# Optimization experiments

Hardware: AMD Instinct MI355X
Metric: run time of the kernel (lower is better)

## Reference

```python
import jax, jax.numpy as jnp
import numpy as np

# Ragged layout: 8 sequences packed into total_tokens=6144 tokens.
_SEQLENS = [1024, 512, 1024, 256, 768, 1024, 512, 1024]
_TOTAL = sum(_SEQLENS)  # 6144
_H, _D = 16, 128
_MAXLEN = 1024


def setup_inputs() -> dict:
    key = jax.random.key(0)
    kq, kk, kv = jax.random.split(key, 3)
    cu = jnp.asarray(np.concatenate([[0], np.cumsum(_SEQLENS)]), dtype=jnp.int32)
    return {
        "q": jax.random.normal(kq, (_TOTAL, _H, _D), dtype=jnp.float32),
        "k": jax.random.normal(kk, (_TOTAL, _H, _D), dtype=jnp.float32),
        "v": jax.random.normal(kv, (_TOTAL, _H, _D), dtype=jnp.float32),
        "cu_seqlens_q": cu,
        "cu_seqlens_k": cu,
        "max_seqlen_q": _MAXLEN,
        "max_seqlen_k": _MAXLEN,
    }


def _pad_gather(x, cu, L):
    """Gather packed [T,h,d] into padded [B,L,h,d] plus validity mask [B,L]."""
    starts = cu[:-1]                                   # [B]
    lens = cu[1:] - cu[:-1]                            # [B]
    pos = jnp.arange(L, dtype=cu.dtype)                # [L]
    idx = starts[:, None] + pos[None, :]               # [B,L]
    mask = pos[None, :] < lens[:, None]                # [B,L]
    idx = jnp.clip(idx, 0, x.shape[0] - 1)
    return x[idx], mask, jnp.where(mask, idx, x.shape[0])


def reference(q, k, v, cu_seqlens_q, cu_seqlens_k, max_seqlen_q, max_seqlen_k):
    # Equivalent to pytorch_varlen_attention: per-sequence SDPA (non-causal,
    # no dropout), vectorized via pad-to-max + key masking.
    T, h, d = q.shape
    qp, mq, idx_q = _pad_gather(q, cu_seqlens_q, max_seqlen_q)  # [B,Lq,h,d]
    kp, mk, _ = _pad_gather(k, cu_seqlens_k, max_seqlen_k)      # [B,Lk,h,d]
    vp, _, _ = _pad_gather(v, cu_seqlens_k, max_seqlen_k)

    scale = 1.0 / jnp.sqrt(jnp.asarray(d, dtype=q.dtype))
    scores = jnp.einsum("bqhd,bkhd->bhqk", qp, kp) * scale      # [B,h,Lq,Lk]
    neg = jnp.asarray(jnp.finfo(scores.dtype).min, scores.dtype)
    scores = jnp.where(mk[:, None, None, :], scores, neg)
    attn = jax.nn.softmax(scores, axis=-1)
    out_pad = jnp.einsum("bhqk,bkhd->bqhd", attn, vp)           # [B,Lq,h,d]

    # Scatter valid rows back to packed layout; invalid rows dropped (idx==T).
    out = jnp.zeros((T, h, d), dtype=q.dtype)
    out = out.at[idx_q.reshape(-1)].set(
        out_pad.reshape(-1, h, d), mode="drop")
    return out
```

## Files before the change

### kernel.cpp

```cpp
#include <hip/hip_runtime.h>
#include <hip/hip_bf16.h>
#include <stdint.h>

#define H 16
#define D 128
#define BM 128
#define BN 64
#define NW 4
#define NT 256

typedef __bf16 bf16_t;
typedef bf16_t bf16x8 __attribute__((ext_vector_type(8)));
typedef bf16_t bf16x2 __attribute__((ext_vector_type(2)));
typedef float f32x16 __attribute__((ext_vector_type(16)));

#define MFMA32(a, b, c) __builtin_amdgcn_mfma_f32_32x32x16_bf16(a, b, c, 0, 0, 0)

union FragU { uint32_t w[4]; bf16x8 v; };

static __device__ __forceinline__ uint32_t cvtpk_bf16(float lo, float hi) {
  uint32_t r;
  asm("v_cvt_pk_bf16_f32 %0, %1, %2" : "=v"(r) : "v"(lo), "v"(hi));
  return r;
}

static __device__ __forceinline__ void gld_lds16(const bf16_t* g, bf16_t* l) {
  __builtin_amdgcn_global_load_lds(
      (const __attribute__((address_space(1))) void*)g,
      (__attribute__((address_space(3))) void*)l, 16, 0, 0);
}


__global__ void conv_k(const float* __restrict__ kin, bf16_t* __restrict__ kb, int n8) {
  int i = blockIdx.x * blockDim.x + threadIdx.x;
  int stride = gridDim.x * blockDim.x;
  for (; i < n8; i += stride) {
    const float* p = kin + (size_t)i * 8;
    float4 a = *(const float4*)p, b = *(const float4*)(p + 4);
    bf16x8 w;
    w[0] = (bf16_t)a.x; w[1] = (bf16_t)a.y; w[2] = (bf16_t)a.z; w[3] = (bf16_t)a.w;
    w[4] = (bf16_t)b.x; w[5] = (bf16_t)b.y; w[6] = (bf16_t)b.z; w[7] = (bf16_t)b.w;
    *(bf16x8*)(kb + (size_t)i * 8) = w;
  }
}

__global__ void conv_vt(const float* __restrict__ v, bf16_t* __restrict__ vt,
                        const int* __restrict__ cuk, int nseq) {
  int tile = blockIdx.x, h = blockIdx.y;
  int acc = 0, seq = -1, lt = 0, s0k = 0, Lk = 0;
  for (int s = 0; s < nseq; ++s) {
    int a = cuk[s], b = cuk[s + 1];
    int Ls = b - a;
    int nt = (Ls + 63) / 64;
    if (tile < acc + nt) { seq = s; lt = tile - acc; s0k = a; Lk = Ls; break; }
    acc += nt;
  }
  if (seq < 0) return;
  int kv0 = lt * 64;
  int d = threadIdx.x;
  bf16x8 w[8];
  #pragma unroll
  for (int j = 0; j < 64; ++j) {
    int kv = kv0 + j; if (kv >= Lk) kv = Lk - 1;
    float val = v[((size_t)(s0k + kv) * H + h) * D + d];
    w[j >> 3][j & 7] = (bf16_t)val;
  }
  bf16_t* row = vt + (size_t)s0k * H * D + ((size_t)h * D + d) * Lk + kv0;
  #pragma unroll
  for (int i = 0; i < 8; ++i) *(bf16x8*)(row + i * 8) = w[i];
}


__global__ __launch_bounds__(NT, 2)
void fa_varlen3(const float* __restrict__ q,
                const bf16_t* __restrict__ kb,
                const bf16_t* __restrict__ vt,
                const int* __restrict__ cuq,
                const int* __restrict__ cuk,
                float* __restrict__ out,
                int nseq)
{
  __shared__ alignas(16) bf16_t sK[2][BN * D];
  __shared__ alignas(16) bf16_t sVt[2][D * BN];
  __shared__ float sRed[NW * 32];

  const int tile = blockIdx.x;
  const int h = blockIdx.y;

  int acc = 0, seq = -1, lt = 0, s0q = 0, s0k = 0, Lq = 0, Lk = 0;
  for (int s = 0; s < nseq; ++s) {
    int a = cuq[s], b = cuq[s + 1];
    int Ls = b - a;
    int nt = (Ls + BM - 1) / BM;
    if (tile < acc + nt) {
      seq = s; lt = tile - acc; s0q = a; Lq = Ls;
      s0k = cuk[s]; Lk = cuk[s + 1] - s0k;
      break;
    }
    acc += nt;
  }
  if (seq < 0) return;

  const int q0 = lt * BM;
  const int tid = threadIdx.x;
  const int warp = tid >> 6;
  const int lane = tid & 63;
  const int lq = lane & 31;
  const int hi = lane >> 5;

  const float SC = 0.08838834764831845f * 1.44269504088896340f;

  bf16x8 qf[8];
  {
    int qrow = q0 + warp * 32 + lq; if (qrow >= Lq) qrow = Lq - 1;
    const float* qp = q + ((size_t)(s0q + qrow) * H + h) * D;
    #pragma unroll
    for (int ks = 0; ks < 8; ++ks) {
      const float* p = qp + ks * 16 + hi * 8;
      float4 a = *(const float4*)p, b = *(const float4*)(p + 4);
      bf16x8 r;
      r[0] = (bf16_t)a.x; r[1] = (bf16_t)a.y; r[2] = (bf16_t)a.z; r[3] = (bf16_t)a.w;
      r[4] = (bf16_t)b.x; r[5] = (bf16_t)b.y; r[6] = (bf16_t)b.z; r[7] = (bf16_t)b.w;
      qf[ks] = r;
    }
  }

  const size_t vtSeqBase = (size_t)s0k * H * D + (size_t)h * D * Lk;

  auto STAGE = [&](int tt, int buf) {
    const int kv0s = tt * BN;
    #pragma unroll
    for (int i = 0; i < 4; ++i) {
      int blk = warp * 4 + i;
      int row = blk * 4 + (lane >> 4);
      int pos = lane & 15;
      int kvr = kv0s + row; if (kvr >= Lk) kvr = Lk - 1;
      const bf16_t* src = kb + ((size_t)(s0k + kvr) * H + h) * D + ((pos ^ (row & 7)) << 3);
      gld_lds16(src, &sK[buf][blk * 512 + lane * 8]);
    }
    #pragma unroll
    for (int i = 0; i < 4; ++i) {
      int blk = warp * 4 + i;
      int d = blk * 8 + (lane >> 3);
      int posc = lane & 7;
      int ck = posc ^ (d & 7);
      int kvs = kv0s + ck * 8; if (kvs > Lk - 8) kvs = Lk - 8;
      const bf16_t* src = vt + vtSeqBase + (size_t)d * Lk + kvs;
      gld_lds16(src, &sVt[buf][blk * 512 + lane * 8]);
    }
  };

  f32x16 oacc[4];
  #pragma unroll
  for (int dt = 0; dt < 4; ++dt)
    #pragma unroll
    for (int r = 0; r < 16; ++r) oacc[dt][r] = 0.f;
  float m = -1e30f, l = 0.f;

  const int nkv = (Lk + BN - 1) / BN;

  STAGE(0, 0);
  asm volatile("s_waitcnt vmcnt(0)" ::: "memory");
  __syncthreads();

  for (int t = 0; t < nkv; ++t) {
    const int cur = t & 1;
    const int kv0 = t * BN;
    if (t + 1 < nkv) STAGE(t + 1, cur ^ 1);

    const bf16_t* sKc = sK[cur];
    const bf16_t* sVc = sVt[cur];
    const bool tail = (kv0 + BN > Lk);

    #pragma unroll
    for (int ct = 0; ct < 2; ++ct) {
      f32x16 st;
      #pragma unroll
      for (int r = 0; r < 16; ++r) st[r] = 0.f;
      int krow = ct * 32 + lq;
      __builtin_amdgcn_s_setprio(1);
      #pragma unroll
      for (int ks = 0; ks < 8; ++ks) {
        int pos = (ks * 2 + hi) ^ (krow & 7);
        bf16x8 kf = *(const bf16x8*)&sKc[krow * 128 + (pos << 3)];
        st = MFMA32(kf, qf[ks], st);
      }
      __builtin_amdgcn_s_setprio(0);

      float tmax = -1e30f;
      #pragma unroll
      for (int r = 0; r < 16; ++r) {
        float x = st[r] * SC;
        if (tail) {
          int kvi = kv0 + ct * 32 + (r & 3) + 8 * (r >> 2) + 4 * hi;
          if (kvi >= Lk) x = -1e30f;
        }
        st[r] = x;
        tmax = fmaxf(tmax, x);
      }
      tmax = fmaxf(tmax, __shfl_xor(tmax, 32));
      bool trig = tmax > m + 8.0f;
      float mnew = trig ? tmax : m;
      float alpha = exp2f(m - mnew);
      m = mnew;

      float psum = 0.f;
      #pragma unroll
      for (int r = 0; r < 16; ++r) {
        float e = exp2f(st[r] - m);
        st[r] = e;
        psum += e;
      }
      psum += __shfl_xor(psum, 32);
      l = l * alpha + psum;

      if (__any(alpha != 1.0f)) {
        if (hi == 0) sRed[warp * 32 + lq] = alpha;
        asm volatile("s_waitcnt lgkmcnt(0)" ::: "memory");
        #pragma unroll
        for (int r = 0; r < 16; ++r) {
          float a2 = sRed[warp * 32 + (r & 3) + 8 * (r >> 2) + 4 * hi];
          #pragma unroll
          for (int dt = 0; dt < 4; ++dt) oacc[dt][r] *= a2;
        }
      }

      uint32_t c0 = cvtpk_bf16(st[0],  st[1]),  c1 = cvtpk_bf16(st[2],  st[3]);
      uint32_t c2 = cvtpk_bf16(st[4],  st[5]),  c3 = cvtpk_bf16(st[6],  st[7]);
      uint32_t c4 = cvtpk_bf16(st[8],  st[9]),  c5 = cvtpk_bf16(st[10], st[11]);
      uint32_t c6 = cvtpk_bf16(st[12], st[13]), c7 = cvtpk_bf16(st[14], st[15]);
      { auto rr = __builtin_amdgcn_permlane32_swap(c0, c2, false, false); c0 = rr[0]; c2 = rr[1]; }
      { auto rr = __builtin_amdgcn_permlane32_swap(c1, c3, false, false); c1 = rr[0]; c3 = rr[1]; }
      { auto rr = __builtin_amdgcn_permlane32_swap(c4, c6, false, false); c4 = rr[0]; c6 = rr[1]; }
      { auto rr = __builtin_amdgcn_permlane32_swap(c5, c7, false, false); c5 = rr[0]; c7 = rr[1]; }
      FragU pa, pb;
      pa.w[0] = c0; pa.w[1] = c1; pa.w[2] = c2; pa.w[3] = c3;
      pb.w[0] = c4; pb.w[1] = c5; pb.w[2] = c6; pb.w[3] = c7;

      __builtin_amdgcn_s_setprio(1);
      #pragma unroll
      for (int dt = 0; dt < 4; ++dt) {
        int drow = dt * 32 + lq;
        int pos0 = (ct * 4 + hi) ^ (drow & 7);
        bf16x8 vf0 = *(const bf16x8*)&sVc[drow * 64 + (pos0 << 3)];
        oacc[dt] = MFMA32(pa.v, vf0, oacc[dt]);
        int pos1 = (ct * 4 + 2 + hi) ^ (drow & 7);
        bf16x8 vf1 = *(const bf16x8*)&sVc[drow * 64 + (pos1 << 3)];
        oacc[dt] = MFMA32(pb.v, vf1, oacc[dt]);
      }
      __builtin_amdgcn_s_setprio(0);
    }

    asm volatile("s_waitcnt vmcnt(0)" ::: "memory");
    __syncthreads();
  }

  if (hi == 0) sRed[warp * 32 + lq] = l;
  asm volatile("s_waitcnt lgkmcnt(0)" ::: "memory");
  #pragma unroll
  for (int r = 0; r < 16; ++r) {
    int cr = (r & 3) + 8 * (r >> 2) + 4 * hi;
    int qr = q0 + warp * 32 + cr;
    if (qr < Lq) {
      float rn = 1.0f / sRed[warp * 32 + cr];
      float* op = out + ((size_t)(s0q + qr) * H + h) * D + lq;
      #pragma unroll
      for (int dt = 0; dt < 4; ++dt)
        op[dt * 32] = oacc[dt][r] * rn;
    }
  }
}


__global__ __launch_bounds__(NT, 3)
void fa_varlen2(const float* __restrict__ q,
                const float* __restrict__ k,
                const float* __restrict__ v,
                const int* __restrict__ cuq,
                const int* __restrict__ cuk,
                float* __restrict__ out,
                int nseq)
{
  __shared__ alignas(16) bf16_t sBuf[128 * 128];
  __shared__ float sRed[NW * 32];
  bf16_t* sK  = sBuf;
  bf16_t* sVt = sBuf + 64 * 128;

  const int tile = blockIdx.x;
  const int h = blockIdx.y;

  int acc = 0, seq = -1, lt = 0, s0q = 0, s0k = 0, Lq = 0, Lk = 0;
  for (int s = 0; s < nseq; ++s) {
    int a = cuq[s], b = cuq[s + 1];
    int Ls = b - a;
    int nt = (Ls + BM - 1) / BM;
    if (tile < acc + nt) {
      seq = s; lt = tile - acc; s0q = a; Lq = Ls;
      s0k = cuk[s]; Lk = cuk[s + 1] - s0k;
      break;
    }
    acc += nt;
  }
  if (seq < 0) return;

  const int q0 = lt * BM;
  const int tid = threadIdx.x;
  const int warp = tid >> 6;
  const int lane = tid & 63;
  const int lq = lane & 31;
  const int hi = lane >> 5;

  const float SC = 0.08838834764831845f * 1.44269504088896340f;

  #pragma unroll
  for (int ii = 0; ii < 8; ++ii) {
    int g = tid + ii * NT;
    int row = g >> 4, cc = g & 15;
    int gr = q0 + row; if (gr >= Lq) gr = Lq - 1;
    const float* p = q + ((size_t)(s0q + gr) * H + h) * D + cc * 8;
    float4 f0 = *(const float4*)p;
    float4 f1 = *(const float4*)(p + 4);
    bf16x8 w;
    w[0] = (bf16_t)f0.x; w[1] = (bf16_t)f0.y; w[2] = (bf16_t)f0.z; w[3] = (bf16_t)f0.w;
    w[4] = (bf16_t)f1.x; w[5] = (bf16_t)f1.y; w[6] = (bf16_t)f1.z; w[7] = (bf16_t)f1.w;
    *(bf16x8*)&sBuf[row * 128 + (((cc ^ (row & 7))) << 3)] = w;
  }
  __syncthreads();

  bf16x8 qf[8];
  {
    int row = warp * 32 + lq;
    #pragma unroll
    for (int ks = 0; ks < 8; ++ks) {
      int pos = (ks * 2 + hi) ^ (row & 7);
      qf[ks] = *(const bf16x8*)&sBuf[row * 128 + (pos << 3)];
    }
  }

  f32x16 oacc[4];
  #pragma unroll
  for (int dt = 0; dt < 4; ++dt)
    #pragma unroll
    for (int r = 0; r < 16; ++r) oacc[dt][r] = 0.f;
  float m = -1e30f, l = 0.f;

  const int nkv = (Lk + BN - 1) / BN;
  for (int it = 0; it < nkv; ++it) {
    const int kv0 = it * BN;
    __syncthreads();

    #pragma unroll
    for (int ii = 0; ii < 4; ++ii) {
      int g = tid + ii * NT;
      int row = g >> 4, cc = g & 15;
      int gr = kv0 + row; if (gr >= Lk) gr = Lk - 1;
      const float* p = k + ((size_t)(s0k + gr) * H + h) * D + cc * 8;
      float4 f0 = *(const float4*)p;
      float4 f1 = *(const float4*)(p + 4);
      bf16x8 w;
      w[0] = (bf16_t)f0.x; w[1] = (bf16_t)f0.y; w[2] = (bf16_t)f0.z; w[3] = (bf16_t)f0.w;
      w[4] = (bf16_t)f1.x; w[5] = (bf16_t)f1.y; w[6] = (bf16_t)f1.z; w[7] = (bf16_t)f1.w;
      *(bf16x8*)&sK[row * 128 + (((cc ^ (row & 7))) << 3)] = w;
    }
    {
      int kp = tid & 31;
      int seg = tid >> 5;
      int r0 = kv0 + 2 * kp, r1 = r0 + 1;
      if (r0 >= Lk) r0 = Lk - 1;
      if (r1 >= Lk) r1 = Lk - 1;
      const float* p0 = v + ((size_t)(s0k + r0) * H + h) * D + seg * 16;
      const float* p1 = v + ((size_t)(s0k + r1) * H + h) * D + seg * 16;
      float va[16], vb[16];
      *(float4*)&va[0]  = *(const float4*)p0;
      *(float4*)&va[4]  = *(const float4*)(p0 + 4);
      *(float4*)&va[8]  = *(const float4*)(p0 + 8);
      *(float4*)&va[12] = *(const float4*)(p0 + 12);
      *(float4*)&vb[0]  = *(const float4*)p1;
      *(float4*)&vb[4]  = *(const float4*)(p1 + 4);
      *(float4*)&vb[8]  = *(const float4*)(p1 + 8);
      *(float4*)&vb[12] = *(const float4*)(p1 + 12);
      int kvr = 2 * kp;
      #pragma unroll
      for (int i = 0; i < 16; ++i) {
        int d = seg * 16 + i;
        int pos = (kp >> 2) ^ (d & 7);
        bf16x2 w2; w2[0] = (bf16_t)va[i]; w2[1] = (bf16_t)vb[i];
        *(bf16x2*)&sVt[d * 64 + (pos << 3) + (kvr & 7)] = w2;
      }
    }
    __syncthreads();

    const bool tail = (kv0 + BN > Lk);

    #pragma unroll
    for (int ct = 0; ct < 2; ++ct) {
      f32x16 st;
      #pragma unroll
      for (int r = 0; r < 16; ++r) st[r] = 0.f;
      int krow = ct * 32 + lq;
      #pragma unroll
      for (int ks = 0; ks < 8; ++ks) {
        int pos = (ks * 2 + hi) ^ (krow & 7);
        bf16x8 kf = *(const bf16x8*)&sK[krow * 128 + (pos << 3)];
        st = MFMA32(kf, qf[ks], st);
      }

      float tmax = -1e30f;
      #pragma unroll
      for (int r = 0; r < 16; ++r) {
        float x = st[r] * SC;
        if (tail) {
          int kvi = kv0 + ct * 32 + (r & 3) + 8 * (r >> 2) + 4 * hi;
          if (kvi >= Lk) x = -1e30f;
        }
        st[r] = x;
        tmax = fmaxf(tmax, x);
      }
      tmax = fmaxf(tmax, __shfl_xor(tmax, 32));
      bool trig = tmax > m + 8.0f;
      float mnew = trig ? tmax : m;
      float alpha = exp2f(m - mnew);
      m = mnew;

      float psum = 0.f;
      #pragma unroll
      for (int r = 0; r < 16; ++r) {
        float e = exp2f(st[r] - m);
        st[r] = e;
        psum += e;
      }
      psum += __shfl_xor(psum, 32);
      l = l * alpha + psum;

      if (__any(alpha != 1.0f)) {
        if (hi == 0) sRed[warp * 32 + lq] = alpha;
        asm volatile("s_waitcnt lgkmcnt(0)" ::: "memory");
        #pragma unroll
        for (int r = 0; r < 16; ++r) {
          float a2 = sRed[warp * 32 + (r & 3) + 8 * (r >> 2) + 4 * hi];
          #pragma unroll
          for (int dt = 0; dt < 4; ++dt) oacc[dt][r] *= a2;
        }
      }

      uint32_t c0 = cvtpk_bf16(st[0],  st[1]),  c1 = cvtpk_bf16(st[2],  st[3]);
      uint32_t c2 = cvtpk_bf16(st[4],  st[5]),  c3 = cvtpk_bf16(st[6],  st[7]);
      uint32_t c4 = cvtpk_bf16(st[8],  st[9]),  c5 = cvtpk_bf16(st[10], st[11]);
      uint32_t c6 = cvtpk_bf16(st[12], st[13]), c7 = cvtpk_bf16(st[14], st[15]);
      { auto rr = __builtin_amdgcn_permlane32_swap(c0, c2, false, false); c0 = rr[0]; c2 = rr[1]; }
      { auto rr = __builtin_amdgcn_permlane32_swap(c1, c3, false, false); c1 = rr[0]; c3 = rr[1]; }
      { auto rr = __builtin_amdgcn_permlane32_swap(c4, c6, false, false); c4 = rr[0]; c6 = rr[1]; }
      { auto rr = __builtin_amdgcn_permlane32_swap(c5, c7, false, false); c5 = rr[0]; c7 = rr[1]; }
      FragU pa, pb;
      pa.w[0] = c0; pa.w[1] = c1; pa.w[2] = c2; pa.w[3] = c3;
      pb.w[0] = c4; pb.w[1] = c5; pb.w[2] = c6; pb.w[3] = c7;

      #pragma unroll
      for (int dt = 0; dt < 4; ++dt) {
        int drow = dt * 32 + lq;
        int pos0 = (ct * 4 + hi) ^ (drow & 7);
        bf16x8 vf0 = *(const bf16x8*)&sVt[drow * 64 + (pos0 << 3)];
        oacc[dt] = MFMA32(pa.v, vf0, oacc[dt]);
        int pos1 = (ct * 4 + 2 + hi) ^ (drow & 7);
        bf16x8 vf1 = *(const bf16x8*)&sVt[drow * 64 + (pos1 << 3)];
        oacc[dt] = MFMA32(pb.v, vf1, oacc[dt]);
      }
    }
  }

  if (hi == 0) sRed[warp * 32 + lq] = l;
  asm volatile("s_waitcnt lgkmcnt(0)" ::: "memory");
  #pragma unroll
  for (int r = 0; r < 16; ++r) {
    int cr = (r & 3) + 8 * (r >> 2) + 4 * hi;
    int qr = q0 + warp * 32 + cr;
    if (qr < Lq) {
      float rn = 1.0f / sRed[warp * 32 + cr];
      float* op = out + ((size_t)(s0q + qr) * H + h) * D + lq;
      #pragma unroll
      for (int dt = 0; dt < 4; ++dt)
        op[dt * 32] = oacc[dt][r] * rn;
    }
  }
}

extern "C" void kernel_launch(void* const* d_in, const int* in_sizes, int n_in,
                              void* d_out, int out_size, void* d_ws, size_t ws_size,
                              hipStream_t stream) {
  const float* q = (const float*)d_in[0];
  const float* k = (const float*)d_in[1];
  const float* v = (const float*)d_in[2];
  const int* cuq = (const int*)d_in[3];
  const int* cuk = (const int*)d_in[4];
  float* out = (float*)d_out;

  int total = in_sizes[0] / (H * D);
  int nseq = in_sizes[3] - 1;
  int maxtiles = (total + BM - 1) / BM + nseq;

  size_t needK = (size_t)in_sizes[1] * 2;
  size_t needV = (size_t)in_sizes[2] * 2;

  dim3 grid(maxtiles, H);

  if (ws_size >= needK + needV) {
    bf16_t* kb = (bf16_t*)d_ws;
    bf16_t* vtb = (bf16_t*)((char*)d_ws + needK);

    conv_k<<<1024, 256, 0, stream>>>(k, kb, in_sizes[1] / 8);
    int maxvt = total / 64 + nseq;
    dim3 gvt(maxvt, H);
    conv_vt<<<gvt, 128, 0, stream>>>(v, vtb, cuk, nseq);
    fa_varlen3<<<grid, NT, 0, stream>>>(q, kb, vtb, cuq, cuk, out, nseq);
  } else {
    fa_varlen2<<<grid, NT, 0, stream>>>(q, k, v, cuq, cuk, out, nseq);
  }
}
```

Baseline: 147.0 us.

## Halve KV tile, pre-tile V^T into fragment-ordered blocks, raise occupancy

```diff
diff --git a/kernel.cpp b/kernel.cpp
--- a/kernel.cpp
+++ b/kernel.cpp
@@ -5,7 +5,7 @@
 #define H 16
 #define D 128
 #define BM 128
-#define BN 64
+#define BN 32
 #define NW 4
 #define NT 256
 
@@ -47,13 +47,14 @@
 __global__ void conv_vt(const float* __restrict__ v, bf16_t* __restrict__ vt,
                         const int* __restrict__ cuk, int nseq) {
   int tile = blockIdx.x, h = blockIdx.y;
-  int acc = 0, seq = -1, lt = 0, s0k = 0, Lk = 0;
+  int acc = 0, seq = -1, lt = 0, s0k = 0, Lk = 0, Lkp = 0;
+  size_t vb = 0;
   for (int s = 0; s < nseq; ++s) {
-    int a = cuk[s], b = cuk[s + 1];
-    int Ls = b - a;
-    int nt = (Ls + 63) / 64;
-    if (tile < acc + nt) { seq = s; lt = tile - acc; s0k = a; Lk = Ls; break; }
-    acc += nt;
+    int Ls = cuk[s + 1] - cuk[s];
+    int Lp = (Ls + 31) & ~31;
+    int nt = (Lp + 63) / 64;
+    if (tile < acc + nt) { seq = s; lt = tile - acc; s0k = cuk[s]; Lk = Ls; Lkp = Lp; break; }
+    acc += nt; vb += (size_t)H * D * Lp;
   }
   if (seq < 0) return;
   int kv0 = lt * 64;
@@ -61,18 +62,25 @@
   bf16x8 w[8];
   #pragma unroll
   for (int j = 0; j < 64; ++j) {
-    int kv = kv0 + j; if (kv >= Lk) kv = Lk - 1;
-    float val = v[((size_t)(s0k + kv) * H + h) * D + d];
+    int kv = kv0 + j;
+    int kvc = kv < Lk ? kv : Lk - 1;
+    float val = v[((size_t)(s0k + kvc) * H + h) * D + d];
     w[j >> 3][j & 7] = (bf16_t)val;
   }
-  bf16_t* row = vt + (size_t)s0k * H * D + ((size_t)h * D + d) * Lk + kv0;
-  #pragma unroll
-  for (int i = 0; i < 8; ++i) *(bf16x8*)(row + i * 8) = w[i];
-}
-
-
-__global__ __launch_bounds__(NT, 2)
-void fa_varlen3(const float* __restrict__ q,
+  bf16_t* dstH = vt + vb + (size_t)h * D * Lkp;
+  #pragma unroll
+  for (int i = 0; i < 8; ++i) {
+    int kv = kv0 + i * 8;
+    if (kv < Lkp) {
+      int tt = kv >> 5, c = (kv >> 3) & 3;
+      *(bf16x8*)(dstH + ((size_t)tt * 512 + c * 128 + d) * 8) = w[i];
+    }
+  }
+}
+
+
+__global__ __launch_bounds__(NT, 4)
+void fa_varlen4(const float* __restrict__ q,
                 const bf16_t* __restrict__ kb,
                 const bf16_t* __restrict__ vt,
                 const int* __restrict__ cuq,
@@ -81,23 +89,26 @@
                 int nseq)
 {
   __shared__ alignas(16) bf16_t sK[2][BN * D];
-  __shared__ alignas(16) bf16_t sVt[2][D * BN];
+  __shared__ alignas(16) bf16_t sVt[2][4 * 128 * 8];
   __shared__ float sRed[NW * 32];
 
   const int tile = blockIdx.x;
   const int h = blockIdx.y;
 
-  int acc = 0, seq = -1, lt = 0, s0q = 0, s0k = 0, Lq = 0, Lk = 0;
+  int acc = 0, seq = -1, lt = 0, s0q = 0, s0k = 0, Lq = 0, Lk = 0, Lkp = 0;
+  size_t vb = 0;
   for (int s = 0; s < nseq; ++s) {
     int a = cuq[s], b = cuq[s + 1];
     int Ls = b - a;
     int nt = (Ls + BM - 1) / BM;
+    int Lks = cuk[s + 1] - cuk[s];
+    int Lp = (Lks + 31) & ~31;
     if (tile < acc + nt) {
       seq = s; lt = tile - acc; s0q = a; Lq = Ls;
-      s0k = cuk[s]; Lk = cuk[s + 1] - s0k;
+      s0k = cuk[s]; Lk = Lks; Lkp = Lp;
       break;
     }
-    acc += nt;
+    acc += nt; vb += (size_t)H * D * Lp;
   }
   if (seq < 0) return;
 
@@ -125,28 +136,23 @@
     }
   }
 
-  const size_t vtSeqBase = (size_t)s0k * H * D + (size_t)h * D * Lk;
+  const bf16_t* vsrcH = vt + vb + (size_t)h * D * Lkp;
 
   auto STAGE = [&](int tt, int buf) {
-    const int kv0s = tt * BN;
-    #pragma unroll
-    for (int i = 0; i < 4; ++i) {
-      int blk = warp * 4 + i;
-      int row = blk * 4 + (lane >> 4);
-      int pos = lane & 15;
-      int kvr = kv0s + row; if (kvr >= Lk) kvr = Lk - 1;
-      const bf16_t* src = kb + ((size_t)(s0k + kvr) * H + h) * D + ((pos ^ (row & 7)) << 3);
-      gld_lds16(src, &sK[buf][blk * 512 + lane * 8]);
-    }
-    #pragma unroll
-    for (int i = 0; i < 4; ++i) {
-      int blk = warp * 4 + i;
-      int d = blk * 8 + (lane >> 3);
-      int posc = lane & 7;
-      int ck = posc ^ (d & 7);
-      int kvs = kv0s + ck * 8; if (kvs > Lk - 8) kvs = Lk - 8;
-      const bf16_t* src = vt + vtSeqBase + (size_t)d * Lk + kvs;
-      gld_lds16(src, &sVt[buf][blk * 512 + lane * 8]);
+    const int kvb = tt * BN;
+    #pragma unroll
+    for (int i = 0; i < 2; ++i) {
+      int g = tid + i * NT;
+      int row = g >> 4, cc = g & 15;
+      int kvr = kvb + row; if (kvr >= Lk) kvr = Lk - 1;
+      const bf16_t* src = kb + ((size_t)(s0k + kvr) * H + h) * D + ((cc ^ (row & 7)) << 3);
+      gld_lds16(src, &sK[buf][g * 8]);
+    }
+    const bf16_t* vsrc = vsrcH + (size_t)tt * 4096;
+    #pragma unroll
+    for (int i = 0; i < 2; ++i) {
+      int g = tid + i * NT;
+      gld_lds16(vsrc + g * 8, &sVt[buf][g * 8]);
     }
   };
 
@@ -165,91 +171,85 @@
 
   for (int t = 0; t < nkv; ++t) {
     const int cur = t & 1;
-    const int kv0 = t * BN;
+    const int kvb = t * BN;
     if (t + 1 < nkv) STAGE(t + 1, cur ^ 1);
 
     const bf16_t* sKc = sK[cur];
     const bf16_t* sVc = sVt[cur];
-    const bool tail = (kv0 + BN > Lk);
-
-    #pragma unroll
-    for (int ct = 0; ct < 2; ++ct) {
-      f32x16 st;
-      #pragma unroll
-      for (int r = 0; r < 16; ++r) st[r] = 0.f;
-      int krow = ct * 32 + lq;
-      __builtin_amdgcn_s_setprio(1);
-      #pragma unroll
-      for (int ks = 0; ks < 8; ++ks) {
-        int pos = (ks * 2 + hi) ^ (krow & 7);
-        bf16x8 kf = *(const bf16x8*)&sKc[krow * 128 + (pos << 3)];
-        st = MFMA32(kf, qf[ks], st);
-      }
-      __builtin_amdgcn_s_setprio(0);
-
-      float tmax = -1e30f;
+    const bool tail = (kvb + BN > Lk);
+
+    f32x16 st;
+    #pragma unroll
+    for (int r = 0; r < 16; ++r) st[r] = 0.f;
+    __builtin_amdgcn_s_setprio(1);
+    #pragma unroll
+    for (int ks = 0; ks < 8; ++ks) {
+      int pos = (ks * 2 + hi) ^ (lq & 7);
+      bf16x8 kf = *(const bf16x8*)&sKc[lq * 128 + (pos << 3)];
+      st = MFMA32(kf, qf[ks], st);
+    }
+    __builtin_amdgcn_s_setprio(0);
+
+    float tmax = -1e30f;
+    #pragma unroll
+    for (int r = 0; r < 16; ++r) {
+      float x = st[r] * SC;
+      if (tail) {
+        int kvi = kvb + (r & 3) + 8 * (r >> 2) + 4 * hi;
+        if (kvi >= Lk) x = -1e30f;
+      }
+      st[r] = x;
+      tmax = fmaxf(tmax, x);
+    }
+    tmax = fmaxf(tmax, __shfl_xor(tmax, 32));
+    bool trig = tmax > m + 8.0f;
+    float mnew = trig ? tmax : m;
+    float alpha = exp2f(m - mnew);
+    m = mnew;
+
+    float psum = 0.f;
+    #pragma unroll
+    for (int r = 0; r < 16; ++r) {
+      float e = exp2f(st[r] - m);
+      st[r] = e;
+      psum += e;
+    }
+    psum += __shfl_xor(psum, 32);
+    l = l * alpha + psum;
+
+    if (__any(alpha != 1.0f)) {
+      if (hi == 0) sRed[warp * 32 + lq] = alpha;
+      asm volatile("s_waitcnt lgkmcnt(0)" ::: "memory");
       #pragma unroll
       for (int r = 0; r < 16; ++r) {
-        float x = st[r] * SC;
-        if (tail) {
-          int kvi = kv0 + ct * 32 + (r & 3) + 8 * (r >> 2) + 4 * hi;
-          if (kvi >= Lk) x = -1e30f;
-        }
-        st[r] = x;
-        tmax = fmaxf(tmax, x);
-      }
-      tmax = fmaxf(tmax, __shfl_xor(tmax, 32));
-      bool trig = tmax > m + 8.0f;
-      float mnew = trig ? tmax : m;
-      float alpha = exp2f(m - mnew);
-      m = mnew;
-
-      float psum = 0.f;
-      #pragma unroll
-      for (int r = 0; r < 16; ++r) {
-        float e = exp2f(st[r] - m);
-        st[r] = e;
-        psum += e;
-      }
-      psum += __shfl_xor(psum, 32);
-      l = l * alpha + psum;
-
-      if (__any(alpha != 1.0f)) {
-        if (hi == 0) sRed[warp * 32 + lq] = alpha;
-        asm volatile("s_waitcnt lgkmcnt(0)" ::: "memory");
+        float a2 = sRed[warp * 32 + (r & 3) + 8 * (r >> 2) + 4 * hi];
         #pragma unroll
-        for (int r = 0; r < 16; ++r) {
-          float a2 = sRed[warp * 32 + (r & 3) + 8 * (r >> 2) + 4 * hi];
-          #pragma unroll
-          for (int dt = 0; dt < 4; ++dt) oacc[dt][r] *= a2;
-        }
-      }
-
-      uint32_t c0 = cvtpk_bf16(st[0],  st[1]),  c1 = cvtpk_bf16(st[2],  st[3]);
-      uint32_t c2 = cvtpk_bf16(st[4],  st[5]),  c3 = cvtpk_bf16(st[6],  st[7]);
-      uint32_t c4 = cvtpk_bf16(st[8],  st[9]),  c5 = cvtpk_bf16(st[10], st[11]);
-      uint32_t c6 = cvtpk_bf16(st[12], st[13]), c7 = cvtpk_bf16(st[14], st[15]);
-      { auto rr = __builtin_amdgcn_permlane32_swap(c0, c2, false, false); c0 = rr[0]; c2 = rr[1]; }
-      { auto rr = __builtin_amdgcn_permlane32_swap(c1, c3, false, false); c1 = rr[0]; c3 = rr[1]; }
-      { auto rr = __builtin_amdgcn_permlane32_swap(c4, c6, false, false); c4 = rr[0]; c6 = rr[1]; }
-      { auto rr = __builtin_amdgcn_permlane32_swap(c5, c7, false, false); c5 = rr[0]; c7 = rr[1]; }
-      FragU pa, pb;
-      pa.w[0] = c0; pa.w[1] = c1; pa.w[2] = c2; pa.w[3] = c3;
-      pb.w[0] = c4; pb.w[1] = c5; pb.w[2] = c6; pb.w[3] = c7;
-
-      __builtin_amdgcn_s_setprio(1);
-      #pragma unroll
-      for (int dt = 0; dt < 4; ++dt) {
-        int drow = dt * 32 + lq;
-        int pos0 = (ct * 4 + hi) ^ (drow & 7);
-        bf16x8 vf0 = *(const bf16x8*)&sVc[drow * 64 + (pos0 << 3)];
-        oacc[dt] = MFMA32(pa.v, vf0, oacc[dt]);
-        int pos1 = (ct * 4 + 2 + hi) ^ (drow & 7);
-        bf16x8 vf1 = *(const bf16x8*)&sVc[drow * 64 + (pos1 << 3)];
-        oacc[dt] = MFMA32(pb.v, vf1, oacc[dt]);
-      }
-      __builtin_amdgcn_s_setprio(0);
-    }
+        for (int dt = 0; dt < 4; ++dt) oacc[dt][r] *= a2;
+      }
+    }
+
+    uint32_t c0 = cvtpk_bf16(st[0],  st[1]),  c1 = cvtpk_bf16(st[2],  st[3]);
+    uint32_t c2 = cvtpk_bf16(st[4],  st[5]),  c3 = cvtpk_bf16(st[6],  st[7]);
+    uint32_t c4 = cvtpk_bf16(st[8],  st[9]),  c5 = cvtpk_bf16(st[10], st[11]);
+    uint32_t c6 = cvtpk_bf16(st[12], st[13]), c7 = cvtpk_bf16(st[14], st[15]);
+    { auto rr = __builtin_amdgcn_permlane32_swap(c0, c2, false, false); c0 = rr[0]; c2 = rr[1]; }
+    { auto rr = __builtin_amdgcn_permlane32_swap(c1, c3, false, false); c1 = rr[0]; c3 = rr[1]; }
+    { auto rr = __builtin_amdgcn_permlane32_swap(c4, c6, false, false); c4 = rr[0]; c6 = rr[1]; }
+    { auto rr = __builtin_amdgcn_permlane32_swap(c5, c7, false, false); c5 = rr[0]; c7 = rr[1]; }
+    FragU pa, pb;
+    pa.w[0] = c0; pa.w[1] = c1; pa.w[2] = c2; pa.w[3] = c3;
+    pb.w[0] = c4; pb.w[1] = c5; pb.w[2] = c6; pb.w[3] = c7;
+
+    __builtin_amdgcn_s_setprio(1);
+    #pragma unroll
+    for (int dt = 0; dt < 4; ++dt) {
+      int drow = dt * 32 + lq;
+      bf16x8 vf0 = *(const bf16x8*)&sVc[(hi * 128 + drow) << 3];
+      oacc[dt] = MFMA32(pa.v, vf0, oacc[dt]);
+      bf16x8 vf1 = *(const bf16x8*)&sVc[((2 + hi) * 128 + drow) << 3];
+      oacc[dt] = MFMA32(pb.v, vf1, oacc[dt]);
+    }
+    __builtin_amdgcn_s_setprio(0);
 
     asm volatile("s_waitcnt vmcnt(0)" ::: "memory");
     __syncthreads();
@@ -344,9 +344,9 @@
     for (int r = 0; r < 16; ++r) oacc[dt][r] = 0.f;
   float m = -1e30f, l = 0.f;
 
-  const int nkv = (Lk + BN - 1) / BN;
+  const int nkv = (Lk + 63) / 64;
   for (int it = 0; it < nkv; ++it) {
-    const int kv0 = it * BN;
+    const int kv0 = it * 64;
     __syncthreads();
 
     #pragma unroll
@@ -370,27 +370,27 @@
       if (r1 >= Lk) r1 = Lk - 1;
       const float* p0 = v + ((size_t)(s0k + r0) * H + h) * D + seg * 16;
       const float* p1 = v + ((size_t)(s0k + r1) * H + h) * D + seg * 16;
-      float va[16], vb[16];
+      float va[16], vbf[16];
       *(float4*)&va[0]  = *(const float4*)p0;
       *(float4*)&va[4]  = *(const float4*)(p0 + 4);
       *(float4*)&va[8]  = *(const float4*)(p0 + 8);
       *(float4*)&va[12] = *(const float4*)(p0 + 12);
-      *(float4*)&vb[0]  = *(const float4*)p1;
-      *(float4*)&vb[4]  = *(const float4*)(p1 + 4);
-      *(float4*)&vb[8]  = *(const float4*)(p1 + 8);
-      *(float4*)&vb[12] = *(const float4*)(p1 + 12);
+      *(float4*)&vbf[0]  = *(const float4*)p1;
+      *(float4*)&vbf[4]  = *(const float4*)(p1 + 4);
+      *(float4*)&vbf[8]  = *(const float4*)(p1 + 8);
+      *(float4*)&vbf[12] = *(const float4*)(p1 + 12);
       int kvr = 2 * kp;
       #pragma unroll
       for (int i = 0; i < 16; ++i) {
         int d = seg * 16 + i;
         int pos = (kp >> 2) ^ (d & 7);
-        bf16x2 w2; w2[0] = (bf16_t)va[i]; w2[1] = (bf16_t)vb[i];
+        bf16x2 w2; w2[0] = (bf16_t)va[i]; w2[1] = (bf16_t)vbf[i];
         *(bf16x2*)&sVt[d * 64 + (pos << 3) + (kvr & 7)] = w2;
       }
     }
     __syncthreads();
 
-    const bool tail = (kv0 + BN > Lk);
+    const bool tail = (kv0 + 64 > Lk);
 
     #pragma unroll
     for (int ct = 0; ct < 2; ++ct) {
@@ -499,7 +499,7 @@
   int maxtiles = (total + BM - 1) / BM + nseq;
 
   size_t needK = (size_t)in_sizes[1] * 2;
-  size_t needV = (size_t)in_sizes[2] * 2;
+  size_t needV = (size_t)in_sizes[2] * 2 + (size_t)nseq * 32 * H * D * 2 + 256;
 
   dim3 grid(maxtiles, H);
 
@@ -508,10 +508,10 @@
     bf16_t* vtb = (bf16_t*)((char*)d_ws + needK);
 
     conv_k<<<1024, 256, 0, stream>>>(k, kb, in_sizes[1] / 8);
-    int maxvt = total / 64 + nseq;
+    int maxvt = (total + 63) / 64 + nseq;
     dim3 gvt(maxvt, H);
     conv_vt<<<gvt, 128, 0, stream>>>(v, vtb, cuk, nseq);
-    fa_varlen3<<<grid, NT, 0, stream>>>(q, kb, vtb, cuq, cuk, out, nseq);
+    fa_varlen4<<<grid, NT, 0, stream>>>(q, kb, vtb, cuq, cuk, out, nseq);
   } else {
     fa_varlen2<<<grid, NT, 0, stream>>>(q, k, v, cuq, cuk, out, nseq);
   }
```

Result: slower. 245.5 us (+67.0%).
